# Kernel optimization log

Measured on AMD Instinct MI355X. Metric: run time of the kernel, lower is better.

Reference implementation:

```python
import jax, jax.numpy as jnp
import numpy as np

N_NODES = 100000
N_EDGES = 1600000
D_NODE = 96
D_EDGE = 32
N_GRAPHS = 128
BN_EPS = 1e-5


def setup_inputs() -> dict:
    key = jax.random.key(0)
    ks = jax.random.split(key, 8)
    x = jax.random.normal(ks[0], (N_NODES, D_NODE), dtype=jnp.float32)
    edge_attr = jax.random.normal(ks[1], (N_EDGES, D_EDGE), dtype=jnp.float32)
    edge_index = jax.random.randint(ks[2], (2, N_EDGES), 0, N_NODES, dtype=jnp.int64)
    batch = jnp.sort(jax.random.randint(ks[3], (N_NODES,), 0, N_GRAPHS, dtype=jnp.int64))
    W1 = jax.random.normal(ks[4], (16, D_NODE + D_EDGE), dtype=jnp.float32) * 0.09
    b1 = jax.random.normal(ks[5], (16,), dtype=jnp.float32) * 0.01
    gamma = jnp.ones((16,), dtype=jnp.float32)
    beta = jnp.zeros((16,), dtype=jnp.float32)
    run_mean = jnp.zeros((16,), dtype=jnp.float32)
    run_var = jnp.ones((16,), dtype=jnp.float32)
    W2 = jax.random.normal(ks[6], (1, 16), dtype=jnp.float32) * 0.25
    b2 = jax.random.normal(ks[7], (1,), dtype=jnp.float32) * 0.01
    return {"x": x, "edge_attr": edge_attr, "edge_index": edge_index, "batch": batch,
            "W1": W1, "b1": b1, "gamma": gamma, "beta": beta,
            "run_mean": run_mean, "run_var": run_var, "W2": W2, "b2": b2}


def reference(x, edge_attr, edge_index, batch, W1, b1, gamma, beta, run_mean, run_var, W2, b2):
    src, dst = edge_index[0], edge_index[1]
    # per-edge message: MLP(cat([x_j, edge_attr]))  -- [E, d_node+d_edge]
    msg_in = jnp.concatenate([x[src], edge_attr], axis=1)
    h = msg_in @ W1.T + b1                                  # [E, 16]
    # BatchNorm1d in eval mode (running stats); Dropout is identity in eval
    h = gamma * (h - run_mean) * jax.lax.rsqrt(run_var + BN_EPS) + beta
    h = jax.nn.relu(h)
    msg = h @ W2.T + b2                                     # [E, 1]
    # scatter-add messages to target nodes
    node_out = jax.ops.segment_sum(msg, dst, num_segments=N_NODES)   # [N, 1]
    # global add pool per graph
    pooled = jax.ops.segment_sum(node_out, batch, num_segments=N_GRAPHS)  # [G, 1]
    # mean over feature dim (size 1)
    return jnp.mean(pooled, axis=1)                         # [G]
```

## Files before the change

### kernel.cpp

```cpp
#include <hip/hip_runtime.h>

#define N_NODES 100000
#define N_EDGES 1600000
#define D_NODE 96
#define D_EDGE 32
#define N_GRAPHS 128
#define BN_EPS 1e-5f

#define EDGE_BLOCKS 1024
#define EDGE_THREADS 256

__global__ void prep_kernel(const float* __restrict__ W1, const float* __restrict__ b1,
                            const float* __restrict__ gamma, const float* __restrict__ beta,
                            const float* __restrict__ rmean, const float* __restrict__ rvar,
                            const float* __restrict__ W2, const float* __restrict__ b2,
                            float* __restrict__ w1n, float* __restrict__ w1e,
                            float* __restrict__ cw) {
    int t = threadIdx.x;
    if (t < 16) {
        float A = gamma[t] * rsqrtf(rvar[t] + BN_EPS);
        cw[t] = A * (b1[t] - rmean[t]) + beta[t];
        cw[16 + t] = W2[t];
        for (int j = 0; j < D_NODE; ++j)
            w1n[t * D_NODE + j] = A * W1[t * (D_NODE + D_EDGE) + j];
        for (int j = 0; j < D_EDGE; ++j)
            w1e[t * D_EDGE + j] = A * W1[t * (D_NODE + D_EDGE) + D_NODE + j];
    }
    if (t == 16) cw[32] = b2[0];
}

__global__ __launch_bounds__(256) void node_proj_kernel(const float* __restrict__ x,
                                                        const float* __restrict__ w1n,
                                                        float* __restrict__ y) {
    int n = blockIdx.x * 256 + threadIdx.x;
    if (n >= N_NODES) return;
    const float4* xr = (const float4*)(x + (size_t)n * D_NODE);
    float acc[16];
#pragma unroll
    for (int k = 0; k < 16; ++k) acc[k] = 0.f;
#pragma unroll
    for (int j4 = 0; j4 < D_NODE / 4; ++j4) {
        float4 xv = xr[j4];
#pragma unroll
        for (int k = 0; k < 16; ++k) {
            const float* w = w1n + k * D_NODE + j4 * 4;
            acc[k] += xv.x * w[0] + xv.y * w[1] + xv.z * w[2] + xv.w * w[3];
        }
    }
    float4* yr = (float4*)(y + (size_t)n * 16);
#pragma unroll
    for (int q = 0; q < 4; ++q)
        yr[q] = make_float4(acc[q * 4 + 0], acc[q * 4 + 1], acc[q * 4 + 2], acc[q * 4 + 3]);
}

__global__ __launch_bounds__(EDGE_THREADS) void edge_kernel(
    const float* __restrict__ ea, const int* __restrict__ eidx,
    const int* __restrict__ batch, const float* __restrict__ y,
    const float* __restrict__ w1e, const float* __restrict__ cw,
    float* __restrict__ partials) {
    __shared__ float bins[N_GRAPHS];
    int t = threadIdx.x;
    if (t < N_GRAPHS) bins[t] = 0.f;
    __syncthreads();

    const int* srcp = eidx;
    const int* dstp = eidx + N_EDGES;
    float b2v = cw[32];

    for (int e = blockIdx.x * EDGE_THREADS + t; e < N_EDGES; e += EDGE_BLOCKS * EDGE_THREADS) {
        int s = srcp[e];
        int d = dstp[e];

        const float4* er = (const float4*)(ea + (size_t)e * D_EDGE);
        float4 ev[8];
#pragma unroll
        for (int i = 0; i < 8; ++i) ev[i] = er[i];

        float ya[16];
        const float4* yr = (const float4*)(y + (size_t)s * 16);
#pragma unroll
        for (int q = 0; q < 4; ++q) ((float4*)ya)[q] = yr[q];

        float msg = b2v;
#pragma unroll
        for (int k = 0; k < 16; ++k) {
            float z = 0.f;
#pragma unroll
            for (int i = 0; i < 8; ++i) {
                const float* w = w1e + k * D_EDGE + i * 4;
                z += ev[i].x * w[0] + ev[i].y * w[1] + ev[i].z * w[2] + ev[i].w * w[3];
            }
            float h = z + ya[k] + cw[k];
            msg += fmaxf(h, 0.f) * cw[16 + k];
        }

        int g = batch[d];
        atomicAdd(&bins[g], msg);
    }

    __syncthreads();
    if (t < N_GRAPHS) partials[(size_t)blockIdx.x * N_GRAPHS + t] = bins[t];
}

__global__ __launch_bounds__(256) void reduce_kernel(const float* __restrict__ partials,
                                                     float* __restrict__ out) {
    __shared__ float s[256];
    int g = blockIdx.x;
    float acc = 0.f;
    for (int b = threadIdx.x; b < EDGE_BLOCKS; b += 256)
        acc += partials[(size_t)b * N_GRAPHS + g];
    s[threadIdx.x] = acc;
    __syncthreads();
    for (int w = 128; w > 0; w >>= 1) {
        if (threadIdx.x < w) s[threadIdx.x] += s[threadIdx.x + w];
        __syncthreads();
    }
    if (threadIdx.x == 0) out[g] = s[0];
}

extern "C" void kernel_launch(void* const* d_in, const int* in_sizes, int n_in,
                              void* d_out, int out_size, void* d_ws, size_t ws_size,
                              hipStream_t stream) {
    const float* x     = (const float*)d_in[0];
    const float* ea    = (const float*)d_in[1];
    const int*   eidx  = (const int*)d_in[2];
    const int*   batch = (const int*)d_in[3];
    const float* W1    = (const float*)d_in[4];
    const float* b1    = (const float*)d_in[5];
    const float* gamma = (const float*)d_in[6];
    const float* beta  = (const float*)d_in[7];
    const float* rmean = (const float*)d_in[8];
    const float* rvar  = (const float*)d_in[9];
    const float* W2    = (const float*)d_in[10];
    const float* b2    = (const float*)d_in[11];
    float* out = (float*)d_out;

    float* ws = (float*)d_ws;
    float* w1n      = ws;
    float* w1e      = ws + 1536;
    float* cw       = ws + 2048;
    float* y        = ws + 4096;
    float* partials = ws + 4096 + (size_t)N_NODES * 16;

    prep_kernel<<<1, 64, 0, stream>>>(W1, b1, gamma, beta, rmean, rvar, W2, b2, w1n, w1e, cw);
    node_proj_kernel<<<(N_NODES + 255) / 256, 256, 0, stream>>>(x, w1n, y);
    edge_kernel<<<EDGE_BLOCKS, EDGE_THREADS, 0, stream>>>(ea, eidx, batch, y, w1e, cw, partials);
    reduce_kernel<<<N_GRAPHS, 256, 0, stream>>>(partials, out);
}
```

Before: 392.2 us.

## Use nontemporal streaming loads and fold final reduction into global atomics

Streaming reads of x, edge_attr and edge indices now use nontemporal loads, so single-use data does less damage to the cache holding the gathered y rows. The separate reduce kernel is removed. Each edge block now atomically adds its 128 shared-memory bins straight into the output, which prep_kernel zeroes first. This saves a launch and the partials round trip, but adds global atomic contention and makes float summation order nondeterministic.

```diff
diff --git a/kernel.cpp b/kernel.cpp
--- a/kernel.cpp
+++ b/kernel.cpp
@@ -10,13 +10,16 @@
 #define EDGE_BLOCKS 1024
 #define EDGE_THREADS 256
 
+typedef float f4 __attribute__((ext_vector_type(4)));
+
 __global__ void prep_kernel(const float* __restrict__ W1, const float* __restrict__ b1,
                             const float* __restrict__ gamma, const float* __restrict__ beta,
                             const float* __restrict__ rmean, const float* __restrict__ rvar,
                             const float* __restrict__ W2, const float* __restrict__ b2,
                             float* __restrict__ w1n, float* __restrict__ w1e,
-                            float* __restrict__ cw) {
+                            float* __restrict__ cw, float* __restrict__ out) {
     int t = threadIdx.x;
+    if (t < N_GRAPHS) out[t] = 0.f;
     if (t < 16) {
         float A = gamma[t] * rsqrtf(rvar[t] + BN_EPS);
         cw[t] = A * (b1[t] - rmean[t]) + beta[t];
@@ -34,13 +37,13 @@
                                                         float* __restrict__ y) {
     int n = blockIdx.x * 256 + threadIdx.x;
     if (n >= N_NODES) return;
-    const float4* xr = (const float4*)(x + (size_t)n * D_NODE);
+    const f4* xr = (const f4*)(x + (size_t)n * D_NODE);
     float acc[16];
 #pragma unroll
     for (int k = 0; k < 16; ++k) acc[k] = 0.f;
 #pragma unroll
     for (int j4 = 0; j4 < D_NODE / 4; ++j4) {
-        float4 xv = xr[j4];
+        f4 xv = __builtin_nontemporal_load(xr + j4);
 #pragma unroll
         for (int k = 0; k < 16; ++k) {
             const float* w = w1n + k * D_NODE + j4 * 4;
@@ -57,7 +60,7 @@
     const float* __restrict__ ea, const int* __restrict__ eidx,
     const int* __restrict__ batch, const float* __restrict__ y,
     const float* __restrict__ w1e, const float* __restrict__ cw,
-    float* __restrict__ partials) {
+    float* __restrict__ out) {
     __shared__ float bins[N_GRAPHS];
     int t = threadIdx.x;
     if (t < N_GRAPHS) bins[t] = 0.f;
@@ -68,13 +71,13 @@
     float b2v = cw[32];
 
     for (int e = blockIdx.x * EDGE_THREADS + t; e < N_EDGES; e += EDGE_BLOCKS * EDGE_THREADS) {
-        int s = srcp[e];
-        int d = dstp[e];
+        int s = __builtin_nontemporal_load(srcp + e);
+        int d = __builtin_nontemporal_load(dstp + e);
 
-        const float4* er = (const float4*)(ea + (size_t)e * D_EDGE);
-        float4 ev[8];
+        const f4* er = (const f4*)(ea + (size_t)e * D_EDGE);
+        f4 ev[8];
 #pragma unroll
-        for (int i = 0; i < 8; ++i) ev[i] = er[i];
+        for (int i = 0; i < 8; ++i) ev[i] = __builtin_nontemporal_load(er + i);
 
         float ya[16];
         const float4* yr = (const float4*)(y + (size_t)s * 16);
@@ -99,23 +102,7 @@
     }
 
     __syncthreads();
-    if (t < N_GRAPHS) partials[(size_t)blockIdx.x * N_GRAPHS + t] = bins[t];
-}
-
-__global__ __launch_bounds__(256) void reduce_kernel(const float* __restrict__ partials,
-                                                     float* __restrict__ out) {
-    __shared__ float s[256];
-    int g = blockIdx.x;
-    float acc = 0.f;
-    for (int b = threadIdx.x; b < EDGE_BLOCKS; b += 256)
-        acc += partials[(size_t)b * N_GRAPHS + g];
-    s[threadIdx.x] = acc;
-    __syncthreads();
-    for (int w = 128; w > 0; w >>= 1) {
-        if (threadIdx.x < w) s[threadIdx.x] += s[threadIdx.x + w];
-        __syncthreads();
-    }
-    if (threadIdx.x == 0) out[g] = s[0];
+    if (t < N_GRAPHS) atomicAdd(&out[t], bins[t]);
 }
 
 extern "C" void kernel_launch(void* const* d_in, const int* in_sizes, int n_in,
@@ -136,14 +123,12 @@
     float* out = (float*)d_out;
 
     float* ws = (float*)d_ws;
-    float* w1n      = ws;
-    float* w1e      = ws + 1536;
-    float* cw       = ws + 2048;
-    float* y        = ws + 4096;
-    float* partials = ws + 4096 + (size_t)N_NODES * 16;
+    float* w1n = ws;
+    float* w1e = ws + 1536;
+    float* cw  = ws + 2048;
+    float* y   = ws + 4096;
 
-    prep_kernel<<<1, 64, 0, stream>>>(W1, b1, gamma, beta, rmean, rvar, W2, b2, w1n, w1e, cw);
+    prep_kernel<<<1, 128, 0, stream>>>(W1, b1, gamma, beta, rmean, rvar, W2, b2, w1n, w1e, cw, out);
     node_proj_kernel<<<(N_NODES + 255) / 256, 256, 0, stream>>>(x, w1n, y);
-    edge_kernel<<<EDGE_BLOCKS, EDGE_THREADS, 0, stream>>>(ea, eidx, batch, y, w1e, cw, partials);
-    reduce_kernel<<<N_GRAPHS, 256, 0, stream>>>(partials, out);
+    edge_kernel<<<EDGE_BLOCKS, EDGE_THREADS, 0, stream>>>(ea, eidx, batch, y, w1e, cw, out);
 }
```

Result: slower. 446.0 us (+13.7%).
